# Kernel optimization log

Measured on AMD Instinct MI355X. Metric: run time of the kernel, lower is better.

The kernel has to match this reference:

```python
import jax, jax.numpy as jnp
import numpy as np

N_NODES = 5000
N_EDGES = 160000
HIDDEN = 64

def setup_inputs() -> dict:
    key = jax.random.key(0)
    ks = jax.random.split(key, 12)
    B, T, N, H, E = 2, 12, N_NODES, HIDDEN, N_EDGES
    s = 0.1
    return {
        "x": jax.random.normal(ks[0], (B, T, N), jnp.float32),
        "edge_index": jax.random.randint(ks[1], (2, E), 0, N, jnp.int64),
        "W1": jax.random.normal(ks[2], (1, H), jnp.float32) * s,
        "b1": jax.random.normal(ks[3], (H,), jnp.float32) * s,
        "W2": jax.random.normal(ks[4], (H, H), jnp.float32) * s,
        "b2": jax.random.normal(ks[5], (H,), jnp.float32) * s,
        "W_ih": jax.random.normal(ks[6], (4 * H, H), jnp.float32) * s,
        "W_hh": jax.random.normal(ks[7], (4 * H, H), jnp.float32) * s,
        "b_ih": jax.random.normal(ks[8], (4 * H,), jnp.float32) * s,
        "b_hh": jax.random.normal(ks[9], (4 * H,), jnp.float32) * s,
        "fc_w": jax.random.normal(ks[10], (H, 1), jnp.float32) * s,
        "fc_b": jax.random.normal(ks[11], (1,), jnp.float32) * s,
    }


def reference(x, edge_index, W1, b1, W2, b2, W_ih, W_hh, b_ih, b_hh, fc_w, fc_b):
    B, T, N = x.shape
    H = W_hh.shape[1]
    src, dst = edge_index[0], edge_index[1]
    loop = jnp.arange(N, dtype=src.dtype)
    src_all = jnp.concatenate([src, loop])  # A + I, PyG add_self_loops
    dst_all = jnp.concatenate([dst, loop])
    # symmetric GCN normalization: deg over destination of A+I
    deg = jnp.zeros((N,), x.dtype).at[dst_all].add(1.0)
    dinv = jax.lax.rsqrt(deg)
    enorm = dinv[src_all] * dinv[dst_all]  # [E+N]

    def gcn(h, W, b):  # h: [B, N, Fin] -> [B, N, H]
        hw = jnp.einsum("bnf,fh->bnh", h, W)
        msg = hw[:, src_all, :] * enorm[None, :, None]  # gather + scale
        agg = jnp.zeros_like(hw).at[:, dst_all, :].add(msg)  # scatter-add
        return agg + b

    xs = jnp.moveaxis(x, 1, 0)[..., None]  # [T, B, N, 1]

    def step(carry, xt):
        h, c = carry
        g = gcn(jax.nn.relu(gcn(xt, W1, b1)), W2, b2)  # [B, N, H]
        g = g.reshape(B * N, H)  # each node is an LSTM sequence element
        gates = g @ W_ih.T + b_ih + h @ W_hh.T + b_hh
        i, f, gg, o = jnp.split(gates, 4, axis=-1)  # torch gate order i,f,g,o
        c = jax.nn.sigmoid(f) * c + jax.nn.sigmoid(i) * jnp.tanh(gg)
        h = jax.nn.sigmoid(o) * jnp.tanh(c)
        return (h, c), None

    h0 = jnp.zeros((B * N, H), x.dtype)
    (hT, _), _ = jax.lax.scan(step, (h0, h0), xs)
    out = (hT @ fc_w + fc_b).reshape(B, N)  # per-node prediction, squeezed
    return out
```

## Files before the change

kernel.cpp:

```cpp
#include <hip/hip_runtime.h>

#define N_NODES 5000
#define N_EDGES 160000
#define BATCH 2
#define TSTEPS 12
#define ROWS (BATCH*N_NODES)
#define RB 16
#define NRB (ROWS/RB)

typedef _Float16 half8_t __attribute__((ext_vector_type(8)));
typedef float f32x4 __attribute__((ext_vector_type(4)));

__device__ inline int swz5000(int gid){ return (gid & 7)*625 + (gid >> 3); }

__global__ void k1(const int* __restrict__ ei, int* __restrict__ cnt,
                   const float* __restrict__ W_ih, const float* __restrict__ W_hh,
                   const float* __restrict__ W2,
                   const float* __restrict__ b_ih, const float* __restrict__ b_hh,
                   const float* __restrict__ b2,
                   _Float16* __restrict__ WFB, float* __restrict__ biasP) {
  int bid = blockIdx.x;
  if (bid < 625) {
    int e = bid*256 + threadIdx.x;
    if (e < N_EDGES) atomicAdd(&cnt[ei[N_EDGES + e]], 1);
    return;
  }
  bid -= 625;
  if (bid < 64) {
    #pragma unroll
    for (int h=0; h<2; ++h){
      int e = bid*512 + h*256 + threadIdx.x;
      int kt4 = e >> 13;
      int rem = e & 8191;
      int ct  = rem >> 9;
      int le  = rem & 511;
      int lane = le >> 3, j = le & 7;
      int colP = (ct&3)*64 + (ct>>2)*16 + (lane&15);
      int kk   = (kt4&1)*32 + (lane>>4)*8 + j;
      float v;
      if (kt4 < 2){
        float s = 0.f;
        #pragma unroll 8
        for (int m=0;m<64;m++) s = fmaf(W2[kk*64+m], W_ih[colP*64+m], s);
        v = s;
      } else {
        v = W_hh[colP*64 + kk];
      }
      WFB[e] = (_Float16)v;
    }
    return;
  }
  int jj = threadIdx.x;
  int ct = jj >> 4, c16 = jj & 15;
  int o = (ct&3)*64 + (ct>>2)*16 + c16;
  float s = b_ih[o] + b_hh[o];
  for (int k=0;k<64;k++) s = fmaf(b2[k], W_ih[o*64+k], s);
  biasP[jj] = s;
}

__global__ void k_scan(const int* __restrict__ cnt, int* __restrict__ row_ptr,
                       float* __restrict__ dinv) {
  __shared__ int sums[1024];
  int tid = threadIdx.x;
  constexpr int C = (N_NODES + 1023)/1024;
  int base = tid*C;
  int local[C];
  int s = 0;
  #pragma unroll
  for (int i=0;i<C;i++){ int idx=base+i; int v=(idx<N_NODES)?cnt[idx]:0; local[i]=s; s+=v; }
  sums[tid]=s; __syncthreads();
  for (int off=1; off<1024; off<<=1) {
    int v = sums[tid];
    int add = (tid>=off)? sums[tid-off]:0;
    __syncthreads();
    sums[tid] = v + add;
    __syncthreads();
  }
  int excl = (tid>0)? sums[tid-1]:0;
  #pragma unroll
  for (int i=0;i<C;i++){ int idx=base+i; if(idx<N_NODES) row_ptr[idx]=excl+local[i]; }
  if (tid==0) row_ptr[N_NODES] = sums[1023];
  #pragma unroll
  for (int i=0;i<C;i++){ int idx=base+i; if(idx<N_NODES) dinv[idx]=rsqrtf((float)(cnt[idx]+1)); }
}

__global__ void k2(const int* __restrict__ ei, const int* __restrict__ row_ptr,
                   int* __restrict__ fill, int* __restrict__ csr_src,
                   const float* __restrict__ x, const float* __restrict__ dinv,
                   float* __restrict__ xdT) {
  int bid = blockIdx.x;
  if (bid < 625) {
    int e = bid*256 + threadIdx.x;
    if (e < N_EDGES) {
      int src = ei[e], dst = ei[N_EDGES+e];
      int pos = row_ptr[dst] + atomicAdd(&fill[dst],1);
      csr_src[pos] = src;
    }
    return;
  }
  int i = (bid-625)*256 + threadIdx.x;
  int n = i >> 5, c = i & 31;
  xdT[i] = (c < 24) ? x[c*N_NODES + n] * dinv[n] : 0.f;
}

__global__ void __launch_bounds__(256) k_p(
    const float* __restrict__ xdT,
    const int* __restrict__ row_ptr, const int* __restrict__ csr_src,
    const float* __restrict__ dinv, float* __restrict__ P)
{
  int tid = threadIdx.x;
  int wv = tid >> 6, lane = tid & 63;
  int s8 = lane >> 3, g8 = lane & 7;
  #pragma unroll
  for (int i=0;i<4;i++){
    int n = blockIdx.x*RB + wv*4 + i;
    if (n >= N_NODES) continue;
    int e0 = row_ptr[n], e1 = row_ptr[n+1];
    float ax=0.f, ay=0.f, az=0.f, aw=0.f;
    int e = e0 + s8;
    for (; e + 8 < e1; e += 16){
      int i1 = csr_src[e], i2 = csr_src[e+8];
      float4 v1 = *(const float4*)&xdT[i1*32 + g8*4];
      float4 v2 = *(const float4*)&xdT[i2*32 + g8*4];
      ax += v1.x + v2.x; ay += v1.y + v2.y;
      az += v1.z + v2.z; aw += v1.w + v2.w;
    }
    if (e < e1){
      int i1 = csr_src[e];
      float4 v1 = *(const float4*)&xdT[i1*32 + g8*4];
      ax += v1.x; ay += v1.y; az += v1.z; aw += v1.w;
    }
    #pragma unroll
    for (int m=8; m<=32; m<<=1){
      ax += __shfl_xor(ax, m, 64); ay += __shfl_xor(ay, m, 64);
      az += __shfl_xor(az, m, 64); aw += __shfl_xor(aw, m, 64);
    }
    if (s8 == 0){
      float4 sv = *(const float4*)&xdT[n*32 + g8*4];
      float dn = dinv[n];
      float4 o;
      o.x = dn*(ax + sv.x); o.y = dn*(ay + sv.y);
      o.z = dn*(az + sv.z); o.w = dn*(aw + sv.w);
      *(float4*)&P[n*32 + g8*4] = o;
    }
  }
}

__global__ void __launch_bounds__(256) k_g(
    const float* __restrict__ P, const float* __restrict__ dinv,
    const float* __restrict__ W1, const float* __restrict__ b1,
    _Float16* __restrict__ g)
{
  int id = blockIdx.x*256 + threadIdx.x;
  int nf = id >> 3, g8 = id & 7;
  int tb = nf / N_NODES;
  int n  = nf - tb*N_NODES;
  float p  = P[n*32 + (tb&1)*12 + (tb>>1)];
  float dn = dinv[n];
  half8_t o;
  #pragma unroll
  for (int j=0;j<8;j++)
    o[j] = (_Float16)(dn * fmaxf(fmaf(p, W1[g8*8+j], b1[g8*8+j]), 0.f));
  *(half8_t*)&g[(size_t)nf*64 + g8*8] = o;
}

__global__ void __launch_bounds__(256) k_agg(
    const _Float16* __restrict__ g,
    const int* __restrict__ row_ptr, const int* __restrict__ csr_src,
    const float* __restrict__ dinv, _Float16* __restrict__ agg2)
{
  int tid = threadIdx.x;
  int wk = swz5000(blockIdx.x);
  int tg = wk / 1250;
  int rb = wk % 1250;
  int r0 = rb*8;
  int wv = tid >> 6, lane = tid & 63;
  int s8 = lane >> 3, g8 = lane & 7;
  #pragma unroll
  for (int i=0;i<2;i++){
    int r = r0 + wv*2 + i;
    int b = (r >= N_NODES) ? 1 : 0;
    int n = r - b*N_NODES;
    const _Float16* h0 = g + ((size_t)(6*tg + b))*N_NODES*64;
    const _Float16* h1 = h0 + (size_t)2*N_NODES*64;
    const _Float16* h2 = h1 + (size_t)2*N_NODES*64;
    int e0 = row_ptr[n], e1 = row_ptr[n+1];
    float a0[8] = {0,0,0,0,0,0,0,0};
    float a1[8] = {0,0,0,0,0,0,0,0};
    float a2[8] = {0,0,0,0,0,0,0,0};
    int e = e0 + s8;
    for (; e + 8 < e1; e += 16){
      size_t oA = (size_t)csr_src[e]*64 + g8*8;
      size_t oB = (size_t)csr_src[e+8]*64 + g8*8;
      half8_t uA0 = *(const half8_t*)(h0 + oA);
      half8_t uA1 = *(const half8_t*)(h1 + oA);
      half8_t uA2 = *(const half8_t*)(h2 + oA);
      half8_t uB0 = *(const half8_t*)(h0 + oB);
      half8_t uB1 = *(const half8_t*)(h1 + oB);
      half8_t uB2 = *(const half8_t*)(h2 + oB);
      #pragma unroll
      for (int j=0;j<8;j++){
        a0[j] += (float)uA0[j] + (float)uB0[j];
        a1[j] += (float)uA1[j] + (float)uB1[j];
        a2[j] += (float)uA2[j] + (float)uB2[j];
      }
    }
    if (e < e1){
      size_t oA = (size_t)csr_src[e]*64 + g8*8;
      half8_t uA0 = *(const half8_t*)(h0 + oA);
      half8_t uA1 = *(const half8_t*)(h1 + oA);
      half8_t uA2 = *(const half8_t*)(h2 + oA);
      #pragma unroll
      for (int j=0;j<8;j++){
        a0[j] += (float)uA0[j]; a1[j] += (float)uA1[j]; a2[j] += (float)uA2[j];
      }
    }
    #pragma unroll
    for (int m=8; m<=32; m<<=1){
      #pragma unroll
      for (int j=0;j<8;j++){
        a0[j] += __shfl_xor(a0[j], m, 64);
        a1[j] += __shfl_xor(a1[j], m, 64);
        a2[j] += __shfl_xor(a2[j], m, 64);
      }
    }
    if (s8 == 0){
      size_t so = (size_t)n*64 + g8*8;
      half8_t sv0 = *(const half8_t*)(h0 + so);
      half8_t sv1 = *(const half8_t*)(h1 + so);
      half8_t sv2 = *(const half8_t*)(h2 + so);
      float dn = dinv[n];
      half8_t q0, q1, q2;
      #pragma unroll
      for (int j=0;j<8;j++){
        q0[j] = (_Float16)(dn*(a0[j] + (float)sv0[j]));
        q1[j] = (_Float16)(dn*(a1[j] + (float)sv1[j]));
        q2[j] = (_Float16)(dn*(a2[j] + (float)sv2[j]));
      }
      _Float16* d0 = &agg2[((size_t)(3*tg)*ROWS + r)*64 + g8*8];
      *(half8_t*)d0 = q0;
      *(half8_t*)(d0 + (size_t)ROWS*64)   = q1;
      *(half8_t*)(d0 + (size_t)2*ROWS*64) = q2;
    }
  }
}

__global__ void __launch_bounds__(256) k_lstm(
    const _Float16* __restrict__ agg2,
    const _Float16* __restrict__ WF,
    const float* __restrict__ biasP,
    const float* __restrict__ fc_w, const float* __restrict__ fc_b,
    float* __restrict__ out)
{
  __shared__ _Float16 sH[2][RB][72];
  __shared__ float sRed[4][16];
  int tid = threadIdx.x;
  int r0 = blockIdx.x*RB;
  int wv = tid >> 6, lane = tid & 63;
  int row = lane & 15, kg = lane >> 4;
  int j = wv*16 + row;

  half8_t Wr[4][4];
  #pragma unroll
  for (int kt4=0; kt4<4; ++kt4)
    #pragma unroll
    for (int i=0;i<4;i++)
      Wr[kt4][i] = *(const half8_t*)(WF + ((size_t)(kt4*16 + wv*4 + i))*512 + (size_t)lane*8);

  float bias[4];
  #pragma unroll
  for (int i=0;i<4;i++) bias[i] = biasP[(wv*4+i)*16 + row];

  float creg[4] = {0.f,0.f,0.f,0.f};
  float hn[4]   = {0.f,0.f,0.f,0.f};

  half8_t pa0, pa1;
  {
    const _Float16* base = &agg2[((size_t)(r0 + row))*64 + kg*8];
    pa0 = *(const half8_t*)base;
    pa1 = *(const half8_t*)(base + 32);
  }

  int pb = 0;
  for (int t=0; t<TSTEPS; ++t){
    half8_t Af0 = pa0, Af1 = pa1;
    if (t+1 < TSTEPS){
      const _Float16* base = &agg2[((size_t)(t+1)*ROWS + r0 + row)*64 + kg*8];
      pa0 = *(const half8_t*)base;
      pa1 = *(const half8_t*)(base + 32);
    }
    half8_t Hf0, Hf1;
    if (t > 0){
      Hf0 = *(const half8_t*)&sH[pb][row][kg*8];
      Hf1 = *(const half8_t*)&sH[pb][row][32 + kg*8];
    }
    f32x4 acc[4];
    #pragma unroll
    for (int i=0;i<4;i++){ acc[i][0]=bias[i]; acc[i][1]=bias[i]; acc[i][2]=bias[i]; acc[i][3]=bias[i]; }
    #pragma unroll
    for (int i=0;i<4;i++){
      f32x4 a = acc[i];
      a = __builtin_amdgcn_mfma_f32_16x16x32_f16(Af0, Wr[0][i], a, 0, 0, 0);
      a = __builtin_amdgcn_mfma_f32_16x16x32_f16(Af1, Wr[1][i], a, 0, 0, 0);
      if (t > 0){
        a = __builtin_amdgcn_mfma_f32_16x16x32_f16(Hf0, Wr[2][i], a, 0, 0, 0);
        a = __builtin_amdgcn_mfma_f32_16x16x32_f16(Hf1, Wr[3][i], a, 0, 0, 0);
      }
      acc[i] = a;
    }
    #pragma unroll
    for (int rr=0;rr<4;rr++){
      float gi = acc[0][rr], gf = acc[1][rr], gg = acc[2][rr], go = acc[3][rr];
      float si = 1.f/(1.f + __expf(-gi));
      float sf = 1.f/(1.f + __expf(-gf));
      float so = 1.f/(1.f + __expf(-go));
      float tg = 2.f/(1.f + __expf(-2.f*gg)) - 1.f;
      float cn = sf*creg[rr] + si*tg;
      creg[rr] = cn;
      float tc = 2.f/(1.f + __expf(-2.f*cn)) - 1.f;
      hn[rr] = so*tc;
      sH[pb^1][kg*4+rr][j] = (_Float16)hn[rr];
    }
    __syncthreads();
    pb ^= 1;
  }
  float fw = fc_w[j];
  #pragma unroll
  for (int rr=0;rr<4;rr++){
    float pv = hn[rr]*fw;
    pv += __shfl_xor(pv, 1, 64);
    pv += __shfl_xor(pv, 2, 64);
    pv += __shfl_xor(pv, 4, 64);
    pv += __shfl_xor(pv, 8, 64);
    if (row == 0) sRed[wv][kg*4+rr] = pv;
  }
  __syncthreads();
  if (tid < 16)
    out[r0 + tid] = sRed[0][tid] + sRed[1][tid] + sRed[2][tid] + sRed[3][tid] + fc_b[0];
}

extern "C" void kernel_launch(void* const* d_in, const int* in_sizes, int n_in,
                              void* d_out, int out_size, void* d_ws, size_t ws_size,
                              hipStream_t stream) {
  const float* x    = (const float*)d_in[0];
  const int*   ei   = (const int*)d_in[1];
  const float* W1   = (const float*)d_in[2];
  const float* b1   = (const float*)d_in[3];
  const float* W2   = (const float*)d_in[4];
  const float* b2   = (const float*)d_in[5];
  const float* W_ih = (const float*)d_in[6];
  const float* W_hh = (const float*)d_in[7];
  const float* b_ih = (const float*)d_in[8];
  const float* b_hh = (const float*)d_in[9];
  const float* fc_w = (const float*)d_in[10];
  const float* fc_b = (const float*)d_in[11];
  float* out = (float*)d_out;

  char* ws = (char*)d_ws;
  size_t off = 0;
  auto alloc = [&](size_t bytes)->void* { void* p = ws + off; off += (bytes + 255) & ~255ul; return p; };
  float*     dinv    = (float*)alloc(N_NODES*4);
  int*       cntfill = (int*)alloc(2*N_NODES*4);
  int*       row_ptr = (int*)alloc((N_NODES+1)*4);
  int*       csr_src = (int*)alloc(N_EDGES*4);
  _Float16*  WFB     = (_Float16*)alloc(4*16*512*2);
  float*     biasP   = (float*)alloc(256*4);
  float*     xdT     = (float*)alloc((size_t)N_NODES*32*4);
  float*     P       = (float*)alloc((size_t)N_NODES*32*4);
  _Float16*  g       = (_Float16*)alloc((size_t)TSTEPS*BATCH*N_NODES*64*2);
  _Float16*  agg2    = (_Float16*)alloc((size_t)TSTEPS*ROWS*64*2);

  int* cnt  = cntfill;
  int* fill = cntfill + N_NODES;

  hipMemsetAsync(cntfill, 0, 2*N_NODES*4, stream);

  k1    <<<690, 256, 0, stream>>>(ei, cnt, W_ih, W_hh, W2, b_ih, b_hh, b2, WFB, biasP);
  k_scan<<<1, 1024, 0, stream>>>(cnt, row_ptr, dinv);
  k2    <<<1250, 256, 0, stream>>>(ei, row_ptr, fill, csr_src, x, dinv, xdT);
  k_p   <<<(N_NODES+RB-1)/RB, 256, 0, stream>>>(xdT, row_ptr, csr_src, dinv, P);
  k_g   <<<3750, 256, 0, stream>>>(P, dinv, W1, b1, g);
  k_agg <<<5000, 256, 0, stream>>>(g, row_ptr, csr_src, dinv, agg2);
  k_lstm<<<NRB, 256, 0, stream>>>(agg2, WFB, biasP, fc_w, fc_b, out);
}
```

Before: 133.5 us.

## Fuse first GCN aggregation with feature expansion and interleave batches in gather layout

Merges k_p and k_g into one kernel that keeps per-node aggregated inputs in shared memory and writes the expanded ReLU features directly, dropping the P intermediate and one launch. The g buffer is relaid out as [t][node][batch*64], so both batches of a node sit in one 256-byte row. k_agg then handles one node per wave for both batches at once, halving csr_src index loads and making each gather wider and contiguous. Pairs of neighbours are now added in fp16 before conversion to fp32, which loses a little precision.

```diff
diff --git a/kernel.cpp b/kernel.cpp
--- a/kernel.cpp
+++ b/kernel.cpp
@@ -103,17 +103,24 @@
   xdT[i] = (c < 24) ? x[c*N_NODES + n] * dinv[n] : 0.f;
 }
 
-__global__ void __launch_bounds__(256) k_p(
+__global__ void __launch_bounds__(256) k_pg(
     const float* __restrict__ xdT,
     const int* __restrict__ row_ptr, const int* __restrict__ csr_src,
-    const float* __restrict__ dinv, float* __restrict__ P)
+    const float* __restrict__ dinv,
+    const float* __restrict__ W1, const float* __restrict__ b1,
+    _Float16* __restrict__ g2)
 {
+  __shared__ float sP[RB][26];
+  __shared__ float sW1[64], sb1[64];
   int tid = threadIdx.x;
+  if (tid < 64) { sW1[tid] = W1[tid]; sb1[tid] = b1[tid]; }
   int wv = tid >> 6, lane = tid & 63;
   int s8 = lane >> 3, g8 = lane & 7;
+  int n0 = blockIdx.x*RB;
   #pragma unroll
   for (int i=0;i<4;i++){
-    int n = blockIdx.x*RB + wv*4 + i;
+    int lr = wv*4 + i;
+    int n = n0 + lr;
     if (n >= N_NODES) continue;
     int e0 = row_ptr[n], e1 = row_ptr[n+1];
     float ax=0.f, ay=0.f, az=0.f, aw=0.f;
@@ -135,113 +142,106 @@
       ax += __shfl_xor(ax, m, 64); ay += __shfl_xor(ay, m, 64);
       az += __shfl_xor(az, m, 64); aw += __shfl_xor(aw, m, 64);
     }
-    if (s8 == 0){
+    if (s8 == 0 && g8 < 6){
       float4 sv = *(const float4*)&xdT[n*32 + g8*4];
       float dn = dinv[n];
-      float4 o;
-      o.x = dn*(ax + sv.x); o.y = dn*(ay + sv.y);
-      o.z = dn*(az + sv.z); o.w = dn*(aw + sv.w);
-      *(float4*)&P[n*32 + g8*4] = o;
-    }
-  }
-}
-
-__global__ void __launch_bounds__(256) k_g(
-    const float* __restrict__ P, const float* __restrict__ dinv,
-    const float* __restrict__ W1, const float* __restrict__ b1,
-    _Float16* __restrict__ g)
-{
-  int id = blockIdx.x*256 + threadIdx.x;
-  int nf = id >> 3, g8 = id & 7;
-  int tb = nf / N_NODES;
-  int n  = nf - tb*N_NODES;
-  float p  = P[n*32 + (tb&1)*12 + (tb>>1)];
-  float dn = dinv[n];
-  half8_t o;
-  #pragma unroll
-  for (int j=0;j<8;j++)
-    o[j] = (_Float16)(dn * fmaxf(fmaf(p, W1[g8*8+j], b1[g8*8+j]), 0.f));
-  *(half8_t*)&g[(size_t)nf*64 + g8*8] = o;
+      sP[lr][g8*4+0] = dn*(ax + sv.x);
+      sP[lr][g8*4+1] = dn*(ay + sv.y);
+      sP[lr][g8*4+2] = dn*(az + sv.z);
+      sP[lr][g8*4+3] = dn*(aw + sv.w);
+    }
+  }
+  __syncthreads();
+  for (int u = tid; u < RB*12*16; u += 256){
+    int node = u / 192;
+    int rem  = u - node*192;
+    int t  = rem >> 4;
+    int oc = rem & 15;
+    int b  = oc >> 3, f8 = oc & 7;
+    int n = n0 + node;
+    if (n >= N_NODES) continue;
+    float p  = sP[node][b*12 + t];
+    float dn = dinv[n];
+    half8_t o;
+    #pragma unroll
+    for (int j=0;j<8;j++)
+      o[j] = (_Float16)(dn * fmaxf(fmaf(p, sW1[f8*8+j], sb1[f8*8+j]), 0.f));
+    *(half8_t*)&g2[((size_t)t*N_NODES + n)*128 + oc*8] = o;
+  }
 }
 
 __global__ void __launch_bounds__(256) k_agg(
-    const _Float16* __restrict__ g,
+    const _Float16* __restrict__ g2,
     const int* __restrict__ row_ptr, const int* __restrict__ csr_src,
     const float* __restrict__ dinv, _Float16* __restrict__ agg2)
 {
   int tid = threadIdx.x;
   int wk = swz5000(blockIdx.x);
   int tg = wk / 1250;
-  int rb = wk % 1250;
-  int r0 = rb*8;
+  int nb = wk % 1250;
   int wv = tid >> 6, lane = tid & 63;
-  int s8 = lane >> 3, g8 = lane & 7;
-  #pragma unroll
-  for (int i=0;i<2;i++){
-    int r = r0 + wv*2 + i;
-    int b = (r >= N_NODES) ? 1 : 0;
-    int n = r - b*N_NODES;
-    const _Float16* h0 = g + ((size_t)(6*tg + b))*N_NODES*64;
-    const _Float16* h1 = h0 + (size_t)2*N_NODES*64;
-    const _Float16* h2 = h1 + (size_t)2*N_NODES*64;
-    int e0 = row_ptr[n], e1 = row_ptr[n+1];
-    float a0[8] = {0,0,0,0,0,0,0,0};
-    float a1[8] = {0,0,0,0,0,0,0,0};
-    float a2[8] = {0,0,0,0,0,0,0,0};
-    int e = e0 + s8;
-    for (; e + 8 < e1; e += 16){
-      size_t oA = (size_t)csr_src[e]*64 + g8*8;
-      size_t oB = (size_t)csr_src[e+8]*64 + g8*8;
-      half8_t uA0 = *(const half8_t*)(h0 + oA);
-      half8_t uA1 = *(const half8_t*)(h1 + oA);
-      half8_t uA2 = *(const half8_t*)(h2 + oA);
-      half8_t uB0 = *(const half8_t*)(h0 + oB);
-      half8_t uB1 = *(const half8_t*)(h1 + oB);
-      half8_t uB2 = *(const half8_t*)(h2 + oB);
-      #pragma unroll
-      for (int j=0;j<8;j++){
-        a0[j] += (float)uA0[j] + (float)uB0[j];
-        a1[j] += (float)uA1[j] + (float)uB1[j];
-        a2[j] += (float)uA2[j] + (float)uB2[j];
-      }
-    }
-    if (e < e1){
-      size_t oA = (size_t)csr_src[e]*64 + g8*8;
-      half8_t uA0 = *(const half8_t*)(h0 + oA);
-      half8_t uA1 = *(const half8_t*)(h1 + oA);
-      half8_t uA2 = *(const half8_t*)(h2 + oA);
-      #pragma unroll
-      for (int j=0;j<8;j++){
-        a0[j] += (float)uA0[j]; a1[j] += (float)uA1[j]; a2[j] += (float)uA2[j];
-      }
-    }
-    #pragma unroll
-    for (int m=8; m<=32; m<<=1){
-      #pragma unroll
-      for (int j=0;j<8;j++){
-        a0[j] += __shfl_xor(a0[j], m, 64);
-        a1[j] += __shfl_xor(a1[j], m, 64);
-        a2[j] += __shfl_xor(a2[j], m, 64);
-      }
-    }
-    if (s8 == 0){
-      size_t so = (size_t)n*64 + g8*8;
-      half8_t sv0 = *(const half8_t*)(h0 + so);
-      half8_t sv1 = *(const half8_t*)(h1 + so);
-      half8_t sv2 = *(const half8_t*)(h2 + so);
-      float dn = dinv[n];
-      half8_t q0, q1, q2;
-      #pragma unroll
-      for (int j=0;j<8;j++){
-        q0[j] = (_Float16)(dn*(a0[j] + (float)sv0[j]));
-        q1[j] = (_Float16)(dn*(a1[j] + (float)sv1[j]));
-        q2[j] = (_Float16)(dn*(a2[j] + (float)sv2[j]));
-      }
-      _Float16* d0 = &agg2[((size_t)(3*tg)*ROWS + r)*64 + g8*8];
-      *(half8_t*)d0 = q0;
-      *(half8_t*)(d0 + (size_t)ROWS*64)   = q1;
-      *(half8_t*)(d0 + (size_t)2*ROWS*64) = q2;
-    }
+  int n = nb*4 + wv;
+  int slot = lane >> 4;
+  int l16 = lane & 15;
+  int b = l16 >> 3, f8 = l16 & 7;
+  const _Float16* gA = g2 + (size_t)(3*tg)*N_NODES*128;
+  const size_t slab = (size_t)N_NODES*128;
+  int e0 = row_ptr[n], e1 = row_ptr[n+1];
+  float a0[8]={0,0,0,0,0,0,0,0}, a1[8]={0,0,0,0,0,0,0,0}, a2[8]={0,0,0,0,0,0,0,0};
+  int e = e0 + slot;
+  for (; e + 4 < e1; e += 8){
+    size_t oA = (size_t)csr_src[e]*128 + l16*8;
+    size_t oB = (size_t)csr_src[e+4]*128 + l16*8;
+    half8_t uA0 = *(const half8_t*)(gA + oA);
+    half8_t uB0 = *(const half8_t*)(gA + oB);
+    half8_t uA1 = *(const half8_t*)(gA + slab + oA);
+    half8_t uB1 = *(const half8_t*)(gA + slab + oB);
+    half8_t uA2 = *(const half8_t*)(gA + 2*slab + oA);
+    half8_t uB2 = *(const half8_t*)(gA + 2*slab + oB);
+    half8_t s0 = uA0 + uB0;
+    half8_t s1 = uA1 + uB1;
+    half8_t s2 = uA2 + uB2;
+    #pragma unroll
+    for (int j=0;j<8;j++){
+      a0[j] += (float)s0[j]; a1[j] += (float)s1[j]; a2[j] += (float)s2[j];
+    }
+  }
+  for (; e < e1; e += 4){
+    size_t oA = (size_t)csr_src[e]*128 + l16*8;
+    half8_t uA0 = *(const half8_t*)(gA + oA);
+    half8_t uA1 = *(const half8_t*)(gA + slab + oA);
+    half8_t uA2 = *(const half8_t*)(gA + 2*slab + oA);
+    #pragma unroll
+    for (int j=0;j<8;j++){
+      a0[j] += (float)uA0[j]; a1[j] += (float)uA1[j]; a2[j] += (float)uA2[j];
+    }
+  }
+  #pragma unroll
+  for (int m=16; m<=32; m<<=1){
+    #pragma unroll
+    for (int j=0;j<8;j++){
+      a0[j] += __shfl_xor(a0[j], m, 64);
+      a1[j] += __shfl_xor(a1[j], m, 64);
+      a2[j] += __shfl_xor(a2[j], m, 64);
+    }
+  }
+  if (slot == 0){
+    size_t so = (size_t)n*128 + l16*8;
+    half8_t sv0 = *(const half8_t*)(gA + so);
+    half8_t sv1 = *(const half8_t*)(gA + slab + so);
+    half8_t sv2 = *(const half8_t*)(gA + 2*slab + so);
+    float dn = dinv[n];
+    half8_t q0, q1, q2;
+    #pragma unroll
+    for (int j=0;j<8;j++){
+      q0[j] = (_Float16)(dn*(a0[j] + (float)sv0[j]));
+      q1[j] = (_Float16)(dn*(a1[j] + (float)sv1[j]));
+      q2[j] = (_Float16)(dn*(a2[j] + (float)sv2[j]));
+    }
+    size_t r64 = ((size_t)(3*tg)*ROWS + b*N_NODES + n)*64 + f8*8;
+    *(half8_t*)&agg2[r64] = q0;
+    *(half8_t*)&agg2[r64 + (size_t)ROWS*64]   = q1;
+    *(half8_t*)&agg2[r64 + (size_t)2*ROWS*64] = q2;
   }
 }
 
@@ -366,8 +366,7 @@
   _Float16*  WFB     = (_Float16*)alloc(4*16*512*2);
   float*     biasP   = (float*)alloc(256*4);
   float*     xdT     = (float*)alloc((size_t)N_NODES*32*4);
-  float*     P       = (float*)alloc((size_t)N_NODES*32*4);
-  _Float16*  g       = (_Float16*)alloc((size_t)TSTEPS*BATCH*N_NODES*64*2);
+  _Float16*  g2      = (_Float16*)alloc((size_t)TSTEPS*N_NODES*128*2);
   _Float16*  agg2    = (_Float16*)alloc((size_t)TSTEPS*ROWS*64*2);
 
   int* cnt  = cntfill;
@@ -378,8 +377,7 @@
   k1    <<<690, 256, 0, stream>>>(ei, cnt, W_ih, W_hh, W2, b_ih, b_hh, b2, WFB, biasP);
   k_scan<<<1, 1024, 0, stream>>>(cnt, row_ptr, dinv);
   k2    <<<1250, 256, 0, stream>>>(ei, row_ptr, fill, csr_src, x, dinv, xdT);
-  k_p   <<<(N_NODES+RB-1)/RB, 256, 0, stream>>>(xdT, row_ptr, csr_src, dinv, P);
-  k_g   <<<3750, 256, 0, stream>>>(P, dinv, W1, b1, g);
-  k_agg <<<5000, 256, 0, stream>>>(g, row_ptr, csr_src, dinv, agg2);
+  k_pg  <<<(N_NODES+RB-1)/RB, 256, 0, stream>>>(xdT, row_ptr, csr_src, dinv, W1, b1, g2);
+  k_agg <<<5000, 256, 0, stream>>>(g2, row_ptr, csr_src, dinv, agg2);
   k_lstm<<<NRB, 256, 0, stream>>>(agg2, WFB, biasP, fc_w, fc_b, out);
 }
```

Result: faster. 116.3 us (-12.8%).

## Replace materialized hidden features with sorted-hinge aggregation per node

Applied to the files above, without the earlier changes.

The separate kernels that materialize the first-layer ReLU features and gather-aggregate them are fused into one kernel. Because the first layer has a single input feature, the ReLU of a rank-one affine map is piecewise linear. Each node sorts its neighbours' scalar inputs with a wavefront bitonic sort, builds prefix sums, and binary-searches the hinge threshold per hidden channel. This removes the large intermediate fp16 buffer and its gathers. The cost is per-node sorting and shuffle work, a slow serial fallback for nodes with more than 64 neighbours, and different floating-point rounding.

```diff
diff --git a/kernel.cpp b/kernel.cpp
--- a/kernel.cpp
+++ b/kernel.cpp
@@ -7,11 +7,10 @@
 #define ROWS (BATCH*N_NODES)
 #define RB 16
 #define NRB (ROWS/RB)
+#define BIGP 1e30f
 
 typedef _Float16 half8_t __attribute__((ext_vector_type(8)));
 typedef float f32x4 __attribute__((ext_vector_type(4)));
-
-__device__ inline int swz5000(int gid){ return (gid & 7)*625 + (gid >> 3); }
 
 __global__ void k1(const int* __restrict__ ei, int* __restrict__ cnt,
                    const float* __restrict__ W_ih, const float* __restrict__ W_hh,
@@ -146,102 +145,103 @@
   }
 }
 
-__global__ void __launch_bounds__(256) k_g(
-    const float* __restrict__ P, const float* __restrict__ dinv,
+__global__ void __launch_bounds__(256) k_hinge(
+    const float* __restrict__ P,
+    const int* __restrict__ row_ptr, const int* __restrict__ csr_src,
+    const float* __restrict__ dinv,
     const float* __restrict__ W1, const float* __restrict__ b1,
-    _Float16* __restrict__ g)
+    _Float16* __restrict__ agg2)
 {
-  int id = blockIdx.x*256 + threadIdx.x;
-  int nf = id >> 3, g8 = id & 7;
-  int tb = nf / N_NODES;
-  int n  = nf - tb*N_NODES;
-  float p  = P[n*32 + (tb&1)*12 + (tb>>1)];
+  __shared__ float nP[4][64][28];
+  __shared__ float nW[4][64];
+  __shared__ float sp[4][64];
+  __shared__ float sW[4][64];
+  __shared__ float sWP[4][64];
+  int tid = threadIdx.x;
+  int wv = tid >> 6, lane = tid & 63;
+  int n = blockIdx.x*4 + wv;
+  float w1f = W1[lane], b1f = b1[lane];
   float dn = dinv[n];
-  half8_t o;
-  #pragma unroll
-  for (int j=0;j<8;j++)
-    o[j] = (_Float16)(dn * fmaxf(fmaf(p, W1[g8*8+j], b1[g8*8+j]), 0.f));
-  *(half8_t*)&g[(size_t)nf*64 + g8*8] = o;
-}
-
-__global__ void __launch_bounds__(256) k_agg(
-    const _Float16* __restrict__ g,
-    const int* __restrict__ row_ptr, const int* __restrict__ csr_src,
-    const float* __restrict__ dinv, _Float16* __restrict__ agg2)
-{
-  int tid = threadIdx.x;
-  int wk = swz5000(blockIdx.x);
-  int tg = wk / 1250;
-  int rb = wk % 1250;
-  int r0 = rb*8;
-  int wv = tid >> 6, lane = tid & 63;
-  int s8 = lane >> 3, g8 = lane & 7;
-  #pragma unroll
-  for (int i=0;i<2;i++){
-    int r = r0 + wv*2 + i;
-    int b = (r >= N_NODES) ? 1 : 0;
-    int n = r - b*N_NODES;
-    const _Float16* h0 = g + ((size_t)(6*tg + b))*N_NODES*64;
-    const _Float16* h1 = h0 + (size_t)2*N_NODES*64;
-    const _Float16* h2 = h1 + (size_t)2*N_NODES*64;
-    int e0 = row_ptr[n], e1 = row_ptr[n+1];
-    float a0[8] = {0,0,0,0,0,0,0,0};
-    float a1[8] = {0,0,0,0,0,0,0,0};
-    float a2[8] = {0,0,0,0,0,0,0,0};
-    int e = e0 + s8;
-    for (; e + 8 < e1; e += 16){
-      size_t oA = (size_t)csr_src[e]*64 + g8*8;
-      size_t oB = (size_t)csr_src[e+8]*64 + g8*8;
-      half8_t uA0 = *(const half8_t*)(h0 + oA);
-      half8_t uA1 = *(const half8_t*)(h1 + oA);
-      half8_t uA2 = *(const half8_t*)(h2 + oA);
-      half8_t uB0 = *(const half8_t*)(h0 + oB);
-      half8_t uB1 = *(const half8_t*)(h1 + oB);
-      half8_t uB2 = *(const half8_t*)(h2 + oB);
+  int e0 = row_ptr[n], e1 = row_ptr[n+1];
+  int deg = e1 - e0;
+
+  if (deg <= 64 && lane < deg){
+    int s = csr_src[e0 + lane];
+    nW[wv][lane] = dinv[s];
+    const float* pr = &P[s*32];
+    #pragma unroll
+    for (int q=0;q<6;q++){
+      float4 v = *(const float4*)(pr + q*4);
+      *(float4*)&nP[wv][lane][q*4] = v;
+    }
+  }
+  __syncthreads();
+
+  if (deg > 64){
+    for (int c=0;c<24;++c){
+      float S = 0.f;
+      for (int e=e0; e<e1; ++e){
+        int s = csr_src[e];
+        float ps = P[s*32 + c];
+        S += dinv[s]*fmaxf(fmaf(w1f, ps, b1f), 0.f);
+      }
+      float pself = P[n*32 + c];
+      S += dn*fmaxf(fmaf(w1f, pself, b1f), 0.f);
+      int b = c/12, t = c - b*12;
+      agg2[((size_t)t*ROWS + b*N_NODES + n)*64 + lane] = (_Float16)(dn*S);
+    }
+    return;
+  }
+
+  for (int c=0; c<24; ++c){
+    float p = (lane < deg) ? nP[wv][lane][c] : BIGP;
+    float w = (lane < deg) ? nW[wv][lane] : 0.f;
+    int idx = lane;
+    #pragma unroll
+    for (int k=2; k<=64; k<<=1){
       #pragma unroll
-      for (int j=0;j<8;j++){
-        a0[j] += (float)uA0[j] + (float)uB0[j];
-        a1[j] += (float)uA1[j] + (float)uB1[j];
-        a2[j] += (float)uA2[j] + (float)uB2[j];
-      }
-    }
-    if (e < e1){
-      size_t oA = (size_t)csr_src[e]*64 + g8*8;
-      half8_t uA0 = *(const half8_t*)(h0 + oA);
-      half8_t uA1 = *(const half8_t*)(h1 + oA);
-      half8_t uA2 = *(const half8_t*)(h2 + oA);
+      for (int j=k>>1; j>0; j>>=1){
+        float p2 = __shfl_xor(p, j, 64);
+        float w2 = __shfl_xor(w, j, 64);
+        int   i2 = __shfl_xor(idx, j, 64);
+        bool takeMin = (((lane & j) == 0) == ((lane & k) == 0));
+        bool less = (p2 < p) || ((p2 == p) && (i2 < idx));
+        bool pick = (less == takeMin);
+        p = pick ? p2 : p;
+        w = pick ? w2 : w;
+        idx = pick ? i2 : idx;
+      }
+    }
+    float Wn = w, WPn = w*p;
+    #pragma unroll
+    for (int d=1; d<64; d<<=1){
+      float tW = __shfl_up(Wn, d, 64);
+      float tP = __shfl_up(WPn, d, 64);
+      if (lane >= d){ Wn += tW; WPn += tP; }
+    }
+    sp[wv][lane] = p; sW[wv][lane] = Wn; sWP[wv][lane] = WPn;
+    float Wtot  = __shfl(Wn, 63, 64);
+    float WPtot = __shfl(WPn, 63, 64);
+    float S;
+    if (w1f != 0.f){
+      float theta = -b1f / w1f;
+      int kk = 0;
       #pragma unroll
-      for (int j=0;j<8;j++){
-        a0[j] += (float)uA0[j]; a1[j] += (float)uA1[j]; a2[j] += (float)uA2[j];
-      }
-    }
-    #pragma unroll
-    for (int m=8; m<=32; m<<=1){
-      #pragma unroll
-      for (int j=0;j<8;j++){
-        a0[j] += __shfl_xor(a0[j], m, 64);
-        a1[j] += __shfl_xor(a1[j], m, 64);
-        a2[j] += __shfl_xor(a2[j], m, 64);
-      }
-    }
-    if (s8 == 0){
-      size_t so = (size_t)n*64 + g8*8;
-      half8_t sv0 = *(const half8_t*)(h0 + so);
-      half8_t sv1 = *(const half8_t*)(h1 + so);
-      half8_t sv2 = *(const half8_t*)(h2 + so);
-      float dn = dinv[n];
-      half8_t q0, q1, q2;
-      #pragma unroll
-      for (int j=0;j<8;j++){
-        q0[j] = (_Float16)(dn*(a0[j] + (float)sv0[j]));
-        q1[j] = (_Float16)(dn*(a1[j] + (float)sv1[j]));
-        q2[j] = (_Float16)(dn*(a2[j] + (float)sv2[j]));
-      }
-      _Float16* d0 = &agg2[((size_t)(3*tg)*ROWS + r)*64 + g8*8];
-      *(half8_t*)d0 = q0;
-      *(half8_t*)(d0 + (size_t)ROWS*64)   = q1;
-      *(half8_t*)(d0 + (size_t)2*ROWS*64) = q2;
-    }
+      for (int st=64; st>0; st>>=1){
+        int t2 = kk + st;
+        if (t2 <= 64 && sp[wv][t2-1] < theta) kk = t2;
+      }
+      float Wb  = (kk>0)? sW[wv][kk-1]  : 0.f;
+      float WPb = (kk>0)? sWP[wv][kk-1] : 0.f;
+      if (w1f > 0.f) S = w1f*(WPtot - WPb) + b1f*(Wtot - Wb);
+      else           S = w1f*WPb + b1f*Wb;
+    } else {
+      S = fmaxf(b1f, 0.f) * Wtot;
+    }
+    float pself = P[n*32 + c];
+    S += dn * fmaxf(fmaf(w1f, pself, b1f), 0.f);
+    int b = c/12, t = c - b*12;
+    agg2[((size_t)t*ROWS + b*N_NODES + n)*64 + lane] = (_Float16)(dn * S);
   }
 }
 
@@ -367,7 +367,6 @@
   float*     biasP   = (float*)alloc(256*4);
   float*     xdT     = (float*)alloc((size_t)N_NODES*32*4);
   float*     P       = (float*)alloc((size_t)N_NODES*32*4);
-  _Float16*  g       = (_Float16*)alloc((size_t)TSTEPS*BATCH*N_NODES*64*2);
   _Float16*  agg2    = (_Float16*)alloc((size_t)TSTEPS*ROWS*64*2);
 
   int* cnt  = cntfill;
@@ -375,11 +374,10 @@
 
   hipMemsetAsync(cntfill, 0, 2*N_NODES*4, stream);
 
-  k1    <<<690, 256, 0, stream>>>(ei, cnt, W_ih, W_hh, W2, b_ih, b_hh, b2, WFB, biasP);
-  k_scan<<<1, 1024, 0, stream>>>(cnt, row_ptr, dinv);
-  k2    <<<1250, 256, 0, stream>>>(ei, row_ptr, fill, csr_src, x, dinv, xdT);
-  k_p   <<<(N_NODES+RB-1)/RB, 256, 0, stream>>>(xdT, row_ptr, csr_src, dinv, P);
-  k_g   <<<3750, 256, 0, stream>>>(P, dinv, W1, b1, g);
-  k_agg <<<5000, 256, 0, stream>>>(g, row_ptr, csr_src, dinv, agg2);
-  k_lstm<<<NRB, 256, 0, stream>>>(agg2, WFB, biasP, fc_w, fc_b, out);
-}
+  k1     <<<690, 256, 0, stream>>>(ei, cnt, W_ih, W_hh, W2, b_ih, b_hh, b2, WFB, biasP);
+  k_scan <<<1, 1024, 0, stream>>>(cnt, row_ptr, dinv);
+  k2     <<<1250, 256, 0, stream>>>(ei, row_ptr, fill, csr_src, x, dinv, xdT);
+  k_p    <<<(N_NODES+RB-1)/RB, 256, 0, stream>>>(xdT, row_ptr, csr_src, dinv, P);
+  k_hinge<<<N_NODES/4, 256, 0, stream>>>(P, row_ptr, csr_src, dinv, W1, b1, agg2);
+  k_lstm <<<NRB, 256, 0, stream>>>(agg2, WFB, biasP, fc_w, fc_b, out);
+}
```

Result: slower. 208.4 us (+56.2%).
